# Kernel tuning notes

Measured on AMD Instinct MI355X. Metric: run time of the kernel, lower is better.

Reference implementation:

```python
import jax, jax.numpy as jnp
import numpy as np

N_NODES = 50000
N_EDGES = 800000
IN_CH = 128
H1, C1 = 8, 16      # conv1: 8 heads x 16 channels, concat -> 128
H2, C2 = 1, 64      # conv2: 1 head x 64 channels, mean (concat=False)
NEG_SLOPE = 0.2


def setup_inputs() -> dict:
    key = jax.random.key(0)
    ks = jax.random.split(key, 10)
    x = jax.random.normal(ks[0], (N_NODES, IN_CH), dtype=jnp.float32)
    edge_index = jax.random.randint(ks[1], (2, N_EDGES), 0, N_NODES, dtype=jnp.int64)
    s1 = 1.0 / np.sqrt(IN_CH)
    s2 = 1.0 / np.sqrt(H1 * C1)
    W1 = jax.random.normal(ks[2], (IN_CH, H1 * C1), dtype=jnp.float32) * s1
    att_src1 = jax.random.normal(ks[3], (H1, C1), dtype=jnp.float32) * s1
    att_dst1 = jax.random.normal(ks[4], (H1, C1), dtype=jnp.float32) * s1
    b1 = jnp.zeros((H1 * C1,), dtype=jnp.float32)
    W2 = jax.random.normal(ks[5], (H1 * C1, H2 * C2), dtype=jnp.float32) * s2
    att_src2 = jax.random.normal(ks[6], (H2, C2), dtype=jnp.float32) * s2
    att_dst2 = jax.random.normal(ks[7], (H2, C2), dtype=jnp.float32) * s2
    b2 = jnp.zeros((C2,), dtype=jnp.float32)
    return {"x": x, "edge_index": edge_index, "W1": W1, "att_src1": att_src1,
            "att_dst1": att_dst1, "b1": b1, "W2": W2, "att_src2": att_src2,
            "att_dst2": att_dst2, "b2": b2}


def gat_conv(x, src, dst, W, att_src, att_dst, bias, heads, out_ch, concat):
    # x: [N, F_in]; src/dst: [E'] (self-loops already appended)
    N = x.shape[0]
    h = (x @ W).reshape(N, heads, out_ch)                     # [N, H, C]
    a_s = jnp.sum(h * att_src[None], axis=-1)                 # [N, H]
    a_d = jnp.sum(h * att_dst[None], axis=-1)                 # [N, H]
    logits = jax.nn.leaky_relu(a_s[src] + a_d[dst], NEG_SLOPE)  # [E', H]
    # segment softmax over edges grouped by destination node
    m = jax.ops.segment_max(logits, dst, num_segments=N)       # [N, H]
    e = jnp.exp(logits - m[dst])                               # [E', H]
    denom = jax.ops.segment_sum(e, dst, num_segments=N)        # [N, H]
    alpha = e / (denom[dst] + 1e-16)                           # [E', H]
    msg = h[src] * alpha[:, :, None]                           # [E', H, C]
    out = jax.ops.segment_sum(msg, dst, num_segments=N)        # [N, H, C]
    if concat:
        out = out.reshape(N, heads * out_ch)
    else:
        out = out.mean(axis=1)
    return out + bias


def reference(x, edge_index, W1, att_src1, att_dst1, b1, W2, att_src2, att_dst2, b2):
    N = x.shape[0]
    loop = jnp.arange(N, dtype=edge_index.dtype)
    src = jnp.concatenate([edge_index[0], loop])   # GATConv adds self-loops
    dst = jnp.concatenate([edge_index[1], loop])
    # eval mode: all dropouts are identity
    h = gat_conv(x, src, dst, W1, att_src1, att_dst1, b1, H1, C1, concat=True)
    h = jax.nn.elu(h)
    out = gat_conv(h, src, dst, W2, att_src2, att_dst2, b2, H2, C2, concat=False)
    return jax.nn.log_softmax(out, axis=1)
```

## Files before the change

kernel.cpp:

```cpp
#include <hip/hip_runtime.h>
#include <math.h>

#define IN_CH 128
#define H1N 8
#define C1N 16
#define C2N 64
#define NEG_SLOPE 0.2f

#define BKT_SHIFT 7
#define BKT_NODES (1 << BKT_SHIFT)
#define NBLK 128

typedef unsigned short ushortT;

__device__ __forceinline__ ushortT f2bf(float f) {
    unsigned u = __float_as_uint(f);
    unsigned r = u + 0x7FFFu + ((u >> 16) & 1u);
    return (ushortT)(r >> 16);
}
__device__ __forceinline__ float bf2f(ushortT b) {
    return __uint_as_float(((unsigned)b) << 16);
}
__device__ __forceinline__ float leaky(float x) {
    return (x > 0.f) ? x : NEG_SLOPE * x;
}


__global__ __launch_bounds__(512) void k_cnt(const int* __restrict__ src,
                                             const int* __restrict__ dst,
                                             int E, int N, int* __restrict__ cnt) {
    __shared__ int hist[512];
    int blk = blockIdx.x, t = threadIdx.x;
    int nb = (N + BKT_NODES - 1) >> BKT_SHIFT;
    if (t < nb) hist[t] = 0;
    __syncthreads();
    int Etot = E + N;
    int chunk = (Etot + gridDim.x - 1) / gridDim.x;
    int lo = blk * chunk;
    int hi = lo + chunk; if (hi > Etot) hi = Etot;
    for (int i = lo + t; i < hi; i += 512) {
        int d = (i < E) ? dst[i] : (i - E);
        atomicAdd(&hist[d >> BKT_SHIFT], 1);
    }
    __syncthreads();
    if (t < nb) cnt[t * NBLK + blk] = hist[t];
}

__global__ __launch_bounds__(NBLK) void k_scanrel(int* __restrict__ cnt,
                                                  int* __restrict__ bucketTotal) {
    __shared__ int sh[NBLK];
    int b = blockIdx.x, t = threadIdx.x;
    sh[t] = cnt[b * NBLK + t];
    __syncthreads();
    for (int off = 1; off < NBLK; off <<= 1) {
        int v = (t >= off) ? sh[t - off] : 0;
        __syncthreads();
        sh[t] += v;
        __syncthreads();
    }
    if (t == NBLK - 1) bucketTotal[b] = sh[t];
    cnt[b * NBLK + t] = (t == 0) ? 0 : sh[t - 1];
}

__global__ __launch_bounds__(512) void k_scanbucket(const int* __restrict__ bucketTotal,
                                                    int nb, int* __restrict__ bBase,
                                                    int N, int* __restrict__ offsets) {
    __shared__ int sh[512];
    int t = threadIdx.x;
    sh[t] = (t < nb) ? bucketTotal[t] : 0;
    __syncthreads();
    for (int off = 1; off < 512; off <<= 1) {
        int v = (t >= off) ? sh[t - off] : 0;
        __syncthreads();
        sh[t] += v;
        __syncthreads();
    }
    if (t < nb) bBase[t] = (t == 0) ? 0 : sh[t - 1];
    if (t == 511) { bBase[nb] = sh[511]; offsets[N] = sh[511]; }
}

__global__ __launch_bounds__(512) void k_bin(const int* __restrict__ src,
                                             const int* __restrict__ dst,
                                             int E, int N,
                                             const int* __restrict__ cnt,
                                             const int* __restrict__ bBase,
                                             unsigned* __restrict__ pair) {
    __shared__ int cur[512];
    int blk = blockIdx.x, t = threadIdx.x;
    int nb = (N + BKT_NODES - 1) >> BKT_SHIFT;
    if (t < nb) cur[t] = bBase[t] + cnt[t * NBLK + blk];
    __syncthreads();
    int Etot = E + N;
    int chunk = (Etot + gridDim.x - 1) / gridDim.x;
    int lo = blk * chunk;
    int hi = lo + chunk; if (hi > Etot) hi = Etot;
    for (int i = lo + t; i < hi; i += 512) {
        int s, d;
        if (i < E) { s = src[i]; d = dst[i]; }
        else       { s = d = i - E; }
        int b = d >> BKT_SHIFT;
        int pos = atomicAdd(&cur[b], 1);
        pair[pos] = ((unsigned)(d & (BKT_NODES - 1)) << 16) | (unsigned)s;
    }
}

__global__ __launch_bounds__(256) void k_csr_local(const unsigned* __restrict__ pair,
                                                   const int* __restrict__ bBase,
                                                   int N, int* __restrict__ offsets,
                                                   ushortT* __restrict__ csr) {
    __shared__ int hist[BKT_NODES];
    __shared__ int loff[BKT_NODES];
    int b = blockIdx.x;
    int t = threadIdx.x;
    int base = bBase[b];
    int cnt = bBase[b + 1] - base;
    const unsigned* pp = pair + base;

    if (t < BKT_NODES) hist[t] = 0;
    __syncthreads();
    for (int i = t; i < cnt; i += 256) atomicAdd(&hist[pp[i] >> 16], 1);
    __syncthreads();
    if (t < BKT_NODES) loff[t] = hist[t];
    __syncthreads();
    for (int off = 1; off < BKT_NODES; off <<= 1) {
        int v = 0;
        if (t < BKT_NODES && t >= off) v = loff[t - off];
        __syncthreads();
        if (t < BKT_NODES) loff[t] += v;
        __syncthreads();
    }
    int node0 = b << BKT_SHIFT;
    if (t < BKT_NODES) {
        int excl = (t == 0) ? 0 : loff[t - 1];
        hist[t] = excl;
        int g = node0 + t;
        if (g < N) offsets[g] = base + excl;
    }
    __syncthreads();
    for (int i = t; i < cnt; i += 256) {
        unsigned pk = pp[i];
        int pos = atomicAdd(&hist[pk >> 16], 1);
        csr[base + pos] = (ushortT)(pk & 0xFFFFu);
    }
}


template <int KOUT, int HEADS>
__global__ __launch_bounds__(256) void k_gemm_att(const float* __restrict__ A,
                                                  const float* __restrict__ W,
                                                  const float* __restrict__ att_s,
                                                  const float* __restrict__ att_d,
                                                  int N, ushortT* __restrict__ Cbf,
                                                  float* __restrict__ as_,
                                                  float* __restrict__ ad_) {
    constexpr int CG  = KOUT / 4;
    constexpr int TY  = 256 / CG;
    constexpr int RPT = 64 / TY;
    constexpr int RW  = (KOUT / HEADS) / 4;
    static_assert(RW == 4 || RW == 16, "reduce width");
    __shared__ float As[64][16];
    __shared__ float Ws[16][KOUT];
    int t = threadIdx.x;
    int row0 = blockIdx.x * 64;
    int tx = t % CG, ty = t / CG;

    float4 acc[RPT];
#pragma unroll
    for (int i = 0; i < RPT; ++i) acc[i] = make_float4(0.f, 0.f, 0.f, 0.f);

    for (int k0 = 0; k0 < IN_CH; k0 += 16) {
        {
            int r  = t >> 2;
            int cc = (t & 3) * 4;
            int gr = row0 + r;
            float4 v = make_float4(0.f, 0.f, 0.f, 0.f);
            if (gr < N) v = *(const float4*)(A + (size_t)gr * IN_CH + k0 + cc);
            *(float4*)(&As[r][cc]) = v;
        }
        {
            constexpr int TOT = 16 * KOUT / 4;
            for (int idx = t; idx < TOT; idx += 256) {
                int rr = idx / (KOUT / 4);
                int cc = (idx % (KOUT / 4)) * 4;
                *(float4*)(&Ws[rr][cc]) = *(const float4*)(W + (size_t)(k0 + rr) * KOUT + cc);
            }
        }
        __syncthreads();
#pragma unroll
        for (int kk = 0; kk < 16; ++kk) {
            float4 w = *(const float4*)(&Ws[kk][tx * 4]);
#pragma unroll
            for (int i = 0; i < RPT; ++i) {
                float a = As[ty * RPT + i][kk];
                acc[i].x += a * w.x; acc[i].y += a * w.y;
                acc[i].z += a * w.z; acc[i].w += a * w.w;
            }
        }
        __syncthreads();
    }

    float4 s4 = *(const float4*)(att_s + tx * 4);
    float4 d4 = *(const float4*)(att_d + tx * 4);
#pragma unroll
    for (int i = 0; i < RPT; ++i) {
        int gr = row0 + ty * RPT + i;
        float as = acc[i].x * s4.x + acc[i].y * s4.y + acc[i].z * s4.z + acc[i].w * s4.w;
        float ad = acc[i].x * d4.x + acc[i].y * d4.y + acc[i].z * d4.z + acc[i].w * d4.w;
#pragma unroll
        for (int o = 1; o < RW; o <<= 1) {
            as += __shfl_xor(as, o);
            ad += __shfl_xor(ad, o);
        }
        if (gr < N) {
            ushort4 pk;
            pk.x = f2bf(acc[i].x); pk.y = f2bf(acc[i].y);
            pk.z = f2bf(acc[i].z); pk.w = f2bf(acc[i].w);
            *(ushort4*)(Cbf + (size_t)gr * KOUT + tx * 4) = pk;
            if ((tx % RW) == 0) {
                int h = tx / RW;
                as_[(size_t)gr * HEADS + h] = as;
                ad_[(size_t)gr * HEADS + h] = ad;
            }
        }
    }
}


__global__ void k_agg1(const ushortT* __restrict__ h1bf,
                       const float* __restrict__ as1, const float* __restrict__ ad1,
                       const int* __restrict__ offsets, const ushortT* __restrict__ csr,
                       const float* __restrict__ b1,
                       int N, float* __restrict__ h2in) {
    int wid  = (blockIdx.x * blockDim.x + threadIdx.x) >> 6;
    int lane = threadIdx.x & 63;
    if (wid >= N) return;
    int v = wid;
    int hc = lane >> 3;
    int hp = lane & 7;
    float adc = ad1[v * H1N + hc];
    float adp = ad1[v * H1N + hp];
    float denom = 0.f, acc0 = 0.f, acc1 = 0.f;
    int beg = offsets[v], end = offsets[v + 1];
    int j = beg;
    for (; j + 8 <= end; j += 8) {
        int ep = lane >> 3;
        int sE = csr[j + ep];
        float a = as1[sE * H1N + hp];
        float pp = __expf(leaky(a + adp));
#pragma unroll
        for (int e = 0; e < 8; ++e) {
            int srcl = e * 8 + hc;
            float pe = __shfl(pp, srcl);
            int   se = __shfl(sE, srcl);
            unsigned q = *(const unsigned*)(h1bf + (size_t)se * IN_CH + lane * 2);
            denom += pe;
            acc0 = fmaf(pe, bf2f((ushortT)(q & 0xFFFFu)), acc0);
            acc1 = fmaf(pe, bf2f((ushortT)(q >> 16)), acc1);
        }
    }
    if (j + 4 <= end) {
        int ep = (lane >> 3) & 3;
        int sE = csr[j + ep];
        float a = as1[sE * H1N + hp];
        float pp = __expf(leaky(a + adp));
#pragma unroll
        for (int e = 0; e < 4; ++e) {
            int srcl = e * 8 + hc;
            float pe = __shfl(pp, srcl);
            int   se = __shfl(sE, srcl);
            unsigned q = *(const unsigned*)(h1bf + (size_t)se * IN_CH + lane * 2);
            denom += pe;
            acc0 = fmaf(pe, bf2f((ushortT)(q & 0xFFFFu)), acc0);
            acc1 = fmaf(pe, bf2f((ushortT)(q >> 16)), acc1);
        }
        j += 4;
    }
    for (; j < end; ++j) {
        int s = csr[j];
        float a = as1[s * H1N + hc];
        unsigned q = *(const unsigned*)(h1bf + (size_t)s * IN_CH + lane * 2);
        float p = __expf(leaky(a + adc));
        denom += p;
        acc0 = fmaf(p, bf2f((ushortT)(q & 0xFFFFu)), acc0);
        acc1 = fmaf(p, bf2f((ushortT)(q >> 16)), acc1);
    }
    float inv = 1.f / (denom + 1e-16f);
    float o0 = acc0 * inv + b1[lane * 2];
    float o1 = acc1 * inv + b1[lane * 2 + 1];
    o0 = (o0 > 0.f) ? o0 : expm1f(o0);
    o1 = (o1 > 0.f) ? o1 : expm1f(o1);
    float2 ov; ov.x = o0; ov.y = o1;
    *(float2*)(h2in + (size_t)v * IN_CH + lane * 2) = ov;
}


__global__ void k_agg2(const ushortT* __restrict__ h2bf,
                       const float* __restrict__ as2, const float* __restrict__ ad2,
                       const int* __restrict__ offsets, const ushortT* __restrict__ csr,
                       const float* __restrict__ b2,
                       int N, float* __restrict__ out) {
    int wid  = (blockIdx.x * blockDim.x + threadIdx.x) >> 6;
    int lane = threadIdx.x & 63;
    if (wid >= N) return;
    int v = wid;
    float ad = ad2[v];
    float denom = 0.f, acc = 0.f;
    int beg = offsets[v], end = offsets[v + 1];
    int j = beg;
    for (; j + 8 <= end; j += 8) {
        int ep = lane & 7;
        int sE = csr[j + ep];
        float pp = __expf(leaky(as2[sE] + ad));
#pragma unroll
        for (int e = 0; e < 8; ++e) {
            float pe = __shfl(pp, e);
            int   se = __shfl(sE, e);
            float x = bf2f(h2bf[(size_t)se * C2N + lane]);
            denom += pe;
            acc = fmaf(pe, x, acc);
        }
    }
    for (; j < end; ++j) {
        int s = csr[j];
        float p = __expf(leaky(as2[s] + ad));
        float x = bf2f(h2bf[(size_t)s * C2N + lane]);
        denom += p;
        acc = fmaf(p, x, acc);
    }
    float o = acc / (denom + 1e-16f) + b2[lane];
    float mx = o;
#pragma unroll
    for (int off = 32; off >= 1; off >>= 1) mx = fmaxf(mx, __shfl_xor(mx, off));
    float e = __expf(o - mx);
    float se = e;
#pragma unroll
    for (int off = 32; off >= 1; off >>= 1) se += __shfl_xor(se, off);
    out[(size_t)v * C2N + lane] = o - mx - logf(se);
}


extern "C" void kernel_launch(void* const* d_in, const int* in_sizes, int n_in,
                              void* d_out, int out_size, void* d_ws, size_t ws_size,
                              hipStream_t stream) {
    const float* x      = (const float*)d_in[0];
    const int*   ei     = (const int*)d_in[1];
    const float* W1     = (const float*)d_in[2];
    const float* att_s1 = (const float*)d_in[3];
    const float* att_d1 = (const float*)d_in[4];
    const float* b1     = (const float*)d_in[5];
    const float* W2     = (const float*)d_in[6];
    const float* att_s2 = (const float*)d_in[7];
    const float* att_d2 = (const float*)d_in[8];
    const float* b2     = (const float*)d_in[9];

    int N = in_sizes[0] / IN_CH;
    int E = in_sizes[1] / 2;
    const int* srcA = ei;
    const int* dstA = ei + E;
    int Etot = E + N;
    int nb = (N + BKT_NODES - 1) >> BKT_SHIFT;

    char* p = (char*)d_ws;
    auto carve = [&](size_t bytes) {
        void* r = (void*)p;
        p += (bytes + 255) & ~(size_t)255;
        return r;
    };
    ushortT* h1bf = (ushortT*)carve((size_t)N * IN_CH * 2);
    ushortT* h2bf = (ushortT*)carve((size_t)N * C2N * 2);
    float* h2in = (float*)carve((size_t)N * IN_CH * 4);
    float* as1  = (float*)carve((size_t)N * H1N * 4);
    float* ad1  = (float*)carve((size_t)N * H1N * 4);
    float* as2  = (float*)carve((size_t)N * 4);
    float* ad2  = (float*)carve((size_t)N * 4);
    int* offsets     = (int*)carve((size_t)(N + 1) * 4);
    ushortT* csr     = (ushortT*)carve((size_t)Etot * 2);
    int* cnt         = (int*)carve((size_t)nb * NBLK * 4);
    int* bucketTotal = (int*)carve((size_t)nb * 4);
    int* bBase       = (int*)carve((size_t)(nb + 1) * 4);
    unsigned* pair   = (unsigned*)carve((size_t)Etot * 4);

    k_cnt<<<NBLK, 512, 0, stream>>>(srcA, dstA, E, N, cnt);
    k_scanrel<<<nb, NBLK, 0, stream>>>(cnt, bucketTotal);
    k_scanbucket<<<1, 512, 0, stream>>>(bucketTotal, nb, bBase, N, offsets);
    k_bin<<<NBLK, 512, 0, stream>>>(srcA, dstA, E, N, cnt, bBase, pair);
    k_csr_local<<<nb, 256, 0, stream>>>(pair, bBase, N, offsets, csr);

    k_gemm_att<128, 8><<<(N + 63) / 64, 256, 0, stream>>>(x, W1, att_s1, att_d1,
                                                          N, h1bf, as1, ad1);
    k_agg1<<<(N * 64 + 255) / 256, 256, 0, stream>>>(h1bf, as1, ad1, offsets, csr, b1, N, h2in);

    k_gemm_att<64, 1><<<(N + 63) / 64, 256, 0, stream>>>(h2in, W2, att_s2, att_d2,
                                                         N, h2bf, as2, ad2);
    k_agg2<<<(N * 64 + 255) / 256, 256, 0, stream>>>(h2bf, as2, ad2, offsets, csr, b2, N, (float*)d_out);
}
```

Before: 164.9 us.

## Split each node's edge aggregation across two wavefronts with LDS combine

```diff
diff --git a/kernel.cpp b/kernel.cpp
--- a/kernel.cpp
+++ b/kernel.cpp
@@ -226,31 +226,41 @@
 }
 
 
-__global__ void k_agg1(const ushortT* __restrict__ h1bf,
+__global__ __launch_bounds__(256) void k_agg1(const ushortT* __restrict__ h1bf,
                        const float* __restrict__ as1, const float* __restrict__ ad1,
                        const int* __restrict__ offsets, const ushortT* __restrict__ csr,
                        const float* __restrict__ b1,
                        int N, float* __restrict__ h2in) {
-    int wid  = (blockIdx.x * blockDim.x + threadIdx.x) >> 6;
-    int lane = threadIdx.x & 63;
-    if (wid >= N) return;
-    int v = wid;
+    __shared__ float comb[2][192];
+    int t = threadIdx.x;
+    int half = t >> 7;
+    int wv   = (t >> 6) & 1;
+    int lane = t & 63;
+    int v = blockIdx.x * 2 + half;
+    bool alive = (v < N);
+
     int hc = lane >> 3;
     int hp = lane & 7;
-    float adc = ad1[v * H1N + hc];
-    float adp = ad1[v * H1N + hp];
+    int ep = lane >> 3;
+    float adp = 0.f;
+    int beg = 0, end = 0;
+    if (alive) {
+        adp = ad1[v * H1N + hp];
+        beg = offsets[v];
+        end = offsets[v + 1];
+    }
     float denom = 0.f, acc0 = 0.f, acc1 = 0.f;
-    int beg = offsets[v], end = offsets[v + 1];
-    int j = beg;
-    for (; j + 8 <= end; j += 8) {
-        int ep = lane >> 3;
-        int sE = csr[j + ep];
-        float a = as1[sE * H1N + hp];
-        float pp = __expf(leaky(a + adp));
-#pragma unroll
-        for (int e = 0; e < 8; ++e) {
+    for (int j = beg + wv * 8; j < end; j += 16) {
+        int m = end - j; if (m > 8) m = 8;
+        int sE = 0;
+        float p = 0.f;
+        if (ep < m) {
+            sE = csr[j + ep];
+            p = __expf(leaky(as1[sE * H1N + hp] + adp));
+        }
+        for (int e = 0; e < m; ++e) {
             int srcl = e * 8 + hc;
-            float pe = __shfl(pp, srcl);
+            float pe = __shfl(p, srcl);
             int   se = __shfl(sE, srcl);
             unsigned q = *(const unsigned*)(h1bf + (size_t)se * IN_CH + lane * 2);
             denom += pe;
@@ -258,84 +268,83 @@
             acc1 = fmaf(pe, bf2f((ushortT)(q >> 16)), acc1);
         }
     }
-    if (j + 4 <= end) {
-        int ep = (lane >> 3) & 3;
-        int sE = csr[j + ep];
-        float a = as1[sE * H1N + hp];
-        float pp = __expf(leaky(a + adp));
-#pragma unroll
-        for (int e = 0; e < 4; ++e) {
-            int srcl = e * 8 + hc;
-            float pe = __shfl(pp, srcl);
-            int   se = __shfl(sE, srcl);
-            unsigned q = *(const unsigned*)(h1bf + (size_t)se * IN_CH + lane * 2);
-            denom += pe;
-            acc0 = fmaf(pe, bf2f((ushortT)(q & 0xFFFFu)), acc0);
-            acc1 = fmaf(pe, bf2f((ushortT)(q >> 16)), acc1);
-        }
-        j += 4;
-    }
-    for (; j < end; ++j) {
-        int s = csr[j];
-        float a = as1[s * H1N + hc];
-        unsigned q = *(const unsigned*)(h1bf + (size_t)s * IN_CH + lane * 2);
-        float p = __expf(leaky(a + adc));
-        denom += p;
-        acc0 = fmaf(p, bf2f((ushortT)(q & 0xFFFFu)), acc0);
-        acc1 = fmaf(p, bf2f((ushortT)(q >> 16)), acc1);
-    }
-    float inv = 1.f / (denom + 1e-16f);
-    float o0 = acc0 * inv + b1[lane * 2];
-    float o1 = acc1 * inv + b1[lane * 2 + 1];
-    o0 = (o0 > 0.f) ? o0 : expm1f(o0);
-    o1 = (o1 > 0.f) ? o1 : expm1f(o1);
-    float2 ov; ov.x = o0; ov.y = o1;
-    *(float2*)(h2in + (size_t)v * IN_CH + lane * 2) = ov;
-}
-
-
-__global__ void k_agg2(const ushortT* __restrict__ h2bf,
+    if (wv == 1) {
+        comb[half][lane * 2]     = acc0;
+        comb[half][lane * 2 + 1] = acc1;
+        comb[half][128 + lane]   = denom;
+    }
+    __syncthreads();
+    if (wv == 0 && alive) {
+        acc0  += comb[half][lane * 2];
+        acc1  += comb[half][lane * 2 + 1];
+        denom += comb[half][128 + lane];
+        float inv = 1.f / (denom + 1e-16f);
+        float o0 = acc0 * inv + b1[lane * 2];
+        float o1 = acc1 * inv + b1[lane * 2 + 1];
+        o0 = (o0 > 0.f) ? o0 : expm1f(o0);
+        o1 = (o1 > 0.f) ? o1 : expm1f(o1);
+        float2 ov; ov.x = o0; ov.y = o1;
+        *(float2*)(h2in + (size_t)v * IN_CH + lane * 2) = ov;
+    }
+}
+
+
+__global__ __launch_bounds__(256) void k_agg2(const ushortT* __restrict__ h2bf,
                        const float* __restrict__ as2, const float* __restrict__ ad2,
                        const int* __restrict__ offsets, const ushortT* __restrict__ csr,
                        const float* __restrict__ b2,
                        int N, float* __restrict__ out) {
-    int wid  = (blockIdx.x * blockDim.x + threadIdx.x) >> 6;
-    int lane = threadIdx.x & 63;
-    if (wid >= N) return;
-    int v = wid;
-    float ad = ad2[v];
+    __shared__ float comb[2][128];
+    int t = threadIdx.x;
+    int half = t >> 7;
+    int wv   = (t >> 6) & 1;
+    int lane = t & 63;
+    int v = blockIdx.x * 2 + half;
+    bool alive = (v < N);
+
+    float ad = 0.f;
+    int beg = 0, end = 0;
+    if (alive) {
+        ad = ad2[v];
+        beg = offsets[v];
+        end = offsets[v + 1];
+    }
     float denom = 0.f, acc = 0.f;
-    int beg = offsets[v], end = offsets[v + 1];
-    int j = beg;
-    for (; j + 8 <= end; j += 8) {
+    for (int j = beg + wv * 8; j < end; j += 16) {
+        int m = end - j; if (m > 8) m = 8;
         int ep = lane & 7;
-        int sE = csr[j + ep];
-        float pp = __expf(leaky(as2[sE] + ad));
-#pragma unroll
-        for (int e = 0; e < 8; ++e) {
-            float pe = __shfl(pp, e);
+        int sE = 0;
+        float p = 0.f;
+        if (ep < m) {
+            sE = csr[j + ep];
+            p = __expf(leaky(as2[sE] + ad));
+        }
+        for (int e = 0; e < m; ++e) {
+            float pe = __shfl(p, e);
             int   se = __shfl(sE, e);
             float x = bf2f(h2bf[(size_t)se * C2N + lane]);
             denom += pe;
             acc = fmaf(pe, x, acc);
         }
     }
-    for (; j < end; ++j) {
-        int s = csr[j];
-        float p = __expf(leaky(as2[s] + ad));
-        float x = bf2f(h2bf[(size_t)s * C2N + lane]);
-        denom += p;
-        acc = fmaf(p, x, acc);
-    }
-    float o = acc / (denom + 1e-16f) + b2[lane];
-    float mx = o;
-#pragma unroll
-    for (int off = 32; off >= 1; off >>= 1) mx = fmaxf(mx, __shfl_xor(mx, off));
-    float e = __expf(o - mx);
-    float se = e;
-#pragma unroll
-    for (int off = 32; off >= 1; off >>= 1) se += __shfl_xor(se, off);
-    out[(size_t)v * C2N + lane] = o - mx - logf(se);
+    if (wv == 1) {
+        comb[half][lane]      = acc;
+        comb[half][64 + lane] = denom;
+    }
+    __syncthreads();
+    if (wv == 0 && alive) {
+        acc   += comb[half][lane];
+        denom += comb[half][64 + lane];
+        float o = acc / (denom + 1e-16f) + b2[lane];
+        float mx = o;
+#pragma unroll
+        for (int off = 32; off >= 1; off >>= 1) mx = fmaxf(mx, __shfl_xor(mx, off));
+        float e = __expf(o - mx);
+        float se = e;
+#pragma unroll
+        for (int off = 32; off >= 1; off >>= 1) se += __shfl_xor(se, off);
+        out[(size_t)v * C2N + lane] = o - mx - logf(se);
+    }
 }
 
 
@@ -388,9 +397,9 @@
 
     k_gemm_att<128, 8><<<(N + 63) / 64, 256, 0, stream>>>(x, W1, att_s1, att_d1,
                                                           N, h1bf, as1, ad1);
-    k_agg1<<<(N * 64 + 255) / 256, 256, 0, stream>>>(h1bf, as1, ad1, offsets, csr, b1, N, h2in);
+    k_agg1<<<(N + 1) / 2, 256, 0, stream>>>(h1bf, as1, ad1, offsets, csr, b1, N, h2in);
 
     k_gemm_att<64, 1><<<(N + 63) / 64, 256, 0, stream>>>(h2in, W2, att_s2, att_d2,
                                                          N, h2bf, as2, ad2);
-    k_agg2<<<(N * 64 + 255) / 256, 256, 0, stream>>>(h2bf, as2, ad2, offsets, csr, b2, N, (float*)d_out);
-}
+    k_agg2<<<(N + 1) / 2, 256, 0, stream>>>(h2bf, as2, ad2, offsets, csr, b2, N, (float*)d_out);
+}
```

Result: slower. 243.7 us (+47.8%).

## Precompute per-edge attention exponentials in separate edge-parallel kernels

Applied to the files above, without the earlier changes.

```diff
diff --git a/kernel.cpp b/kernel.cpp
--- a/kernel.cpp
+++ b/kernel.cpp
@@ -12,6 +12,7 @@
 #define NBLK 128
 
 typedef unsigned short ushortT;
+typedef unsigned char ucharT;
 
 __device__ __forceinline__ ushortT f2bf(float f) {
     unsigned u = __float_as_uint(f);
@@ -107,7 +108,8 @@
 __global__ __launch_bounds__(256) void k_csr_local(const unsigned* __restrict__ pair,
                                                    const int* __restrict__ bBase,
                                                    int N, int* __restrict__ offsets,
-                                                   ushortT* __restrict__ csr) {
+                                                   ushortT* __restrict__ csr,
+                                                   ucharT* __restrict__ dloc) {
     __shared__ int hist[BKT_NODES];
     __shared__ int loff[BKT_NODES];
     int b = blockIdx.x;
@@ -139,8 +141,10 @@
     __syncthreads();
     for (int i = t; i < cnt; i += 256) {
         unsigned pk = pp[i];
-        int pos = atomicAdd(&hist[pk >> 16], 1);
-        csr[base + pos] = (ushortT)(pk & 0xFFFFu);
+        int dl = pk >> 16;
+        int pos = atomicAdd(&hist[dl], 1);
+        csr[base + pos]  = (ushortT)(pk & 0xFFFFu);
+        dloc[base + pos] = (ucharT)dl;
     }
 }
 
@@ -226,63 +230,91 @@
 }
 
 
-__global__ void k_agg1(const ushortT* __restrict__ h1bf,
-                       const float* __restrict__ as1, const float* __restrict__ ad1,
+__global__ __launch_bounds__(256) void k_pexp1(const ushortT* __restrict__ csr,
+                                               const ucharT* __restrict__ dloc,
+                                               const int* __restrict__ bBase,
+                                               const float* __restrict__ as1,
+                                               const float* __restrict__ ad1,
+                                               int N, int Etot,
+                                               ushortT* __restrict__ p1T) {
+    __shared__ float ad1s[BKT_NODES * H1N];
+    int b = blockIdx.x, t = threadIdx.x;
+    int node0 = b << BKT_SHIFT;
+    for (int i = t; i < BKT_NODES * H1N; i += 256) {
+        int g = node0 + (i >> 3);
+        ad1s[i] = (g < N) ? ad1[(size_t)g * H1N + (i & 7)] : 0.f;
+    }
+    __syncthreads();
+    int base = bBase[b];
+    int cnt  = bBase[b + 1] - base;
+#pragma unroll
+    for (int h = 0; h < H1N; ++h) {
+        for (int i = t; i < cnt; i += 256) {
+            int s  = csr[base + i];
+            int dl = dloc[base + i];
+            float a = as1[(size_t)s * H1N + h] + ad1s[dl * H1N + h];
+            p1T[(size_t)h * Etot + base + i] = f2bf(__expf(leaky(a)));
+        }
+    }
+}
+
+__global__ __launch_bounds__(256) void k_pexp2(const ushortT* __restrict__ csr,
+                                               const ucharT* __restrict__ dloc,
+                                               const int* __restrict__ bBase,
+                                               const float* __restrict__ as2,
+                                               const float* __restrict__ ad2,
+                                               int N,
+                                               ushortT* __restrict__ p2) {
+    __shared__ float ad2s[BKT_NODES];
+    int b = blockIdx.x, t = threadIdx.x;
+    int node0 = b << BKT_SHIFT;
+    if (t < BKT_NODES) {
+        int g = node0 + t;
+        ad2s[t] = (g < N) ? ad2[g] : 0.f;
+    }
+    __syncthreads();
+    int base = bBase[b];
+    int cnt  = bBase[b + 1] - base;
+    for (int i = t; i < cnt; i += 256) {
+        int s  = csr[base + i];
+        int dl = dloc[base + i];
+        p2[base + i] = f2bf(__expf(leaky(as2[s] + ad2s[dl])));
+    }
+}
+
+
+__global__ __launch_bounds__(256) void k_agg1(const ushortT* __restrict__ h1bf,
+                       const ushortT* __restrict__ p1T,
                        const int* __restrict__ offsets, const ushortT* __restrict__ csr,
                        const float* __restrict__ b1,
-                       int N, float* __restrict__ h2in) {
+                       int N, int Etot, float* __restrict__ h2in) {
     int wid  = (blockIdx.x * blockDim.x + threadIdx.x) >> 6;
     int lane = threadIdx.x & 63;
     if (wid >= N) return;
     int v = wid;
     int hc = lane >> 3;
-    int hp = lane & 7;
-    float adc = ad1[v * H1N + hc];
-    float adp = ad1[v * H1N + hp];
+    const ushortT* pT = p1T + (size_t)hc * Etot;
     float denom = 0.f, acc0 = 0.f, acc1 = 0.f;
     int beg = offsets[v], end = offsets[v + 1];
     int j = beg;
     for (; j + 8 <= end; j += 8) {
-        int ep = lane >> 3;
-        int sE = csr[j + ep];
-        float a = as1[sE * H1N + hp];
-        float pp = __expf(leaky(a + adp));
 #pragma unroll
         for (int e = 0; e < 8; ++e) {
-            int srcl = e * 8 + hc;
-            float pe = __shfl(pp, srcl);
-            int   se = __shfl(sE, srcl);
+            int se = csr[j + e];
+            float pe = bf2f(pT[j + e]);
             unsigned q = *(const unsigned*)(h1bf + (size_t)se * IN_CH + lane * 2);
             denom += pe;
             acc0 = fmaf(pe, bf2f((ushortT)(q & 0xFFFFu)), acc0);
             acc1 = fmaf(pe, bf2f((ushortT)(q >> 16)), acc1);
         }
     }
-    if (j + 4 <= end) {
-        int ep = (lane >> 3) & 3;
-        int sE = csr[j + ep];
-        float a = as1[sE * H1N + hp];
-        float pp = __expf(leaky(a + adp));
-#pragma unroll
-        for (int e = 0; e < 4; ++e) {
-            int srcl = e * 8 + hc;
-            float pe = __shfl(pp, srcl);
-            int   se = __shfl(sE, srcl);
-            unsigned q = *(const unsigned*)(h1bf + (size_t)se * IN_CH + lane * 2);
-            denom += pe;
-            acc0 = fmaf(pe, bf2f((ushortT)(q & 0xFFFFu)), acc0);
-            acc1 = fmaf(pe, bf2f((ushortT)(q >> 16)), acc1);
-        }
-        j += 4;
-    }
     for (; j < end; ++j) {
-        int s = csr[j];
-        float a = as1[s * H1N + hc];
-        unsigned q = *(const unsigned*)(h1bf + (size_t)s * IN_CH + lane * 2);
-        float p = __expf(leaky(a + adc));
-        denom += p;
-        acc0 = fmaf(p, bf2f((ushortT)(q & 0xFFFFu)), acc0);
-        acc1 = fmaf(p, bf2f((ushortT)(q >> 16)), acc1);
+        int se = csr[j];
+        float pe = bf2f(pT[j]);
+        unsigned q = *(const unsigned*)(h1bf + (size_t)se * IN_CH + lane * 2);
+        denom += pe;
+        acc0 = fmaf(pe, bf2f((ushortT)(q & 0xFFFFu)), acc0);
+        acc1 = fmaf(pe, bf2f((ushortT)(q >> 16)), acc1);
     }
     float inv = 1.f / (denom + 1e-16f);
     float o0 = acc0 * inv + b1[lane * 2];
@@ -294,8 +326,8 @@
 }
 
 
-__global__ void k_agg2(const ushortT* __restrict__ h2bf,
-                       const float* __restrict__ as2, const float* __restrict__ ad2,
+__global__ __launch_bounds__(256) void k_agg2(const ushortT* __restrict__ h2bf,
+                       const ushortT* __restrict__ p2,
                        const int* __restrict__ offsets, const ushortT* __restrict__ csr,
                        const float* __restrict__ b2,
                        int N, float* __restrict__ out) {
@@ -303,29 +335,25 @@
     int lane = threadIdx.x & 63;
     if (wid >= N) return;
     int v = wid;
-    float ad = ad2[v];
     float denom = 0.f, acc = 0.f;
     int beg = offsets[v], end = offsets[v + 1];
     int j = beg;
     for (; j + 8 <= end; j += 8) {
-        int ep = lane & 7;
-        int sE = csr[j + ep];
-        float pp = __expf(leaky(as2[sE] + ad));
 #pragma unroll
         for (int e = 0; e < 8; ++e) {
-            float pe = __shfl(pp, e);
-            int   se = __shfl(sE, e);
+            int se = csr[j + e];
+            float pe = bf2f(p2[j + e]);
             float x = bf2f(h2bf[(size_t)se * C2N + lane]);
             denom += pe;
             acc = fmaf(pe, x, acc);
         }
     }
     for (; j < end; ++j) {
-        int s = csr[j];
-        float p = __expf(leaky(as2[s] + ad));
-        float x = bf2f(h2bf[(size_t)s * C2N + lane]);
-        denom += p;
-        acc = fmaf(p, x, acc);
+        int se = csr[j];
+        float pe = bf2f(p2[j]);
+        float x = bf2f(h2bf[(size_t)se * C2N + lane]);
+        denom += pe;
+        acc = fmaf(pe, x, acc);
     }
     float o = acc / (denom + 1e-16f) + b2[lane];
     float mx = o;
@@ -375,22 +403,29 @@
     float* ad2  = (float*)carve((size_t)N * 4);
     int* offsets     = (int*)carve((size_t)(N + 1) * 4);
     ushortT* csr     = (ushortT*)carve((size_t)Etot * 2);
+    ucharT* dloc     = (ucharT*)carve((size_t)Etot);
     int* cnt         = (int*)carve((size_t)nb * NBLK * 4);
     int* bucketTotal = (int*)carve((size_t)nb * 4);
     int* bBase       = (int*)carve((size_t)(nb + 1) * 4);
     unsigned* pair   = (unsigned*)carve((size_t)Etot * 4);
+    ushortT* p1T     = (ushortT*)carve((size_t)H1N * Etot * 2);
+    ushortT* p2      = (ushortT*)carve((size_t)Etot * 2);
 
     k_cnt<<<NBLK, 512, 0, stream>>>(srcA, dstA, E, N, cnt);
     k_scanrel<<<nb, NBLK, 0, stream>>>(cnt, bucketTotal);
     k_scanbucket<<<1, 512, 0, stream>>>(bucketTotal, nb, bBase, N, offsets);
     k_bin<<<NBLK, 512, 0, stream>>>(srcA, dstA, E, N, cnt, bBase, pair);
-    k_csr_local<<<nb, 256, 0, stream>>>(pair, bBase, N, offsets, csr);
+    k_csr_local<<<nb, 256, 0, stream>>>(pair, bBase, N, offsets, csr, dloc);
 
     k_gemm_att<128, 8><<<(N + 63) / 64, 256, 0, stream>>>(x, W1, att_s1, att_d1,
                                                           N, h1bf, as1, ad1);
-    k_agg1<<<(N * 64 + 255) / 256, 256, 0, stream>>>(h1bf, as1, ad1, offsets, csr, b1, N, h2in);
+    k_pexp1<<<nb, 256, 0, stream>>>(csr, dloc, bBase, as1, ad1, N, Etot, p1T);
+    k_agg1<<<(N * 64 + 255) / 256, 256, 0, stream>>>(h1bf, p1T, offsets, csr, b1,
+                                                     N, Etot, h2in);
 
     k_gemm_att<64, 1><<<(N + 63) / 64, 256, 0, stream>>>(h2in, W2, att_s2, att_d2,
                                                          N, h2bf, as2, ad2);
-    k_agg2<<<(N * 64 + 255) / 256, 256, 0, stream>>>(h2bf, as2, ad2, offsets, csr, b2, N, (float*)d_out);
-}
+    k_pexp2<<<nb, 256, 0, stream>>>(csr, dloc, bBase, as2, ad2, N, p2);
+    k_agg2<<<(N * 64 + 255) / 256, 256, 0, stream>>>(h2bf, p2, offsets, csr, b2,
+                                                     N, (float*)d_out);
+}
```

New measurement: 214.7 us. 1.3x slower.

## Store layer-1 output in bf16 and process two nodes per wavefront in agg2

Applied to the files above, without the earlier changes.

```diff
diff --git a/kernel.cpp b/kernel.cpp
--- a/kernel.cpp
+++ b/kernel.cpp
@@ -145,8 +145,8 @@
 }
 
 
-template <int KOUT, int HEADS>
-__global__ __launch_bounds__(256) void k_gemm_att(const float* __restrict__ A,
+template <int KOUT, int HEADS, bool BFIN>
+__global__ __launch_bounds__(256) void k_gemm_att(const void* __restrict__ Av,
                                                   const float* __restrict__ W,
                                                   const float* __restrict__ att_s,
                                                   const float* __restrict__ att_d,
@@ -174,7 +174,16 @@
             int cc = (t & 3) * 4;
             int gr = row0 + r;
             float4 v = make_float4(0.f, 0.f, 0.f, 0.f);
-            if (gr < N) v = *(const float4*)(A + (size_t)gr * IN_CH + k0 + cc);
+            if (gr < N) {
+                if constexpr (BFIN) {
+                    const ushortT* A = (const ushortT*)Av;
+                    ushort4 u = *(const ushort4*)(A + (size_t)gr * IN_CH + k0 + cc);
+                    v.x = bf2f(u.x); v.y = bf2f(u.y); v.z = bf2f(u.z); v.w = bf2f(u.w);
+                } else {
+                    const float* A = (const float*)Av;
+                    v = *(const float4*)(A + (size_t)gr * IN_CH + k0 + cc);
+                }
+            }
             *(float4*)(&As[r][cc]) = v;
         }
         {
@@ -230,7 +239,7 @@
                        const float* __restrict__ as1, const float* __restrict__ ad1,
                        const int* __restrict__ offsets, const ushortT* __restrict__ csr,
                        const float* __restrict__ b1,
-                       int N, float* __restrict__ h2in) {
+                       int N, ushortT* __restrict__ h2in) {
     int wid  = (blockIdx.x * blockDim.x + threadIdx.x) >> 6;
     int lane = threadIdx.x & 63;
     if (wid >= N) return;
@@ -289,53 +298,79 @@
     float o1 = acc1 * inv + b1[lane * 2 + 1];
     o0 = (o0 > 0.f) ? o0 : expm1f(o0);
     o1 = (o1 > 0.f) ? o1 : expm1f(o1);
-    float2 ov; ov.x = o0; ov.y = o1;
-    *(float2*)(h2in + (size_t)v * IN_CH + lane * 2) = ov;
-}
-
-
-__global__ void k_agg2(const ushortT* __restrict__ h2bf,
+    unsigned pk = ((unsigned)f2bf(o1) << 16) | (unsigned)f2bf(o0);
+    *(unsigned*)(h2in + (size_t)v * IN_CH + lane * 2) = pk;
+}
+
+
+__global__ __launch_bounds__(256) void k_agg2(const ushortT* __restrict__ h2bf,
                        const float* __restrict__ as2, const float* __restrict__ ad2,
                        const int* __restrict__ offsets, const ushortT* __restrict__ csr,
                        const float* __restrict__ b2,
                        int N, float* __restrict__ out) {
     int wid  = (blockIdx.x * blockDim.x + threadIdx.x) >> 6;
     int lane = threadIdx.x & 63;
-    if (wid >= N) return;
-    int v = wid;
-    float ad = ad2[v];
-    float denom = 0.f, acc = 0.f;
-    int beg = offsets[v], end = offsets[v + 1];
+    int half = lane >> 5;
+    int v = wid * 2 + half;
+    bool alive = (v < N);
+    int c2 = (lane & 31) * 2;
+
+    float ad = 0.f;
+    int beg = 0, end = 0;
+    if (alive) {
+        ad = ad2[v];
+        beg = offsets[v];
+        end = offsets[v + 1];
+    }
+    float denom = 0.f, acc0 = 0.f, acc1 = 0.f;
     int j = beg;
     for (; j + 8 <= end; j += 8) {
+        int sE = csr[j + (lane & 7)];
+        float p = __expf(leaky(as2[sE] + ad));
+#pragma unroll
+        for (int e = 0; e < 8; ++e) {
+            int srcl = (lane & 32) + e;
+            float pe = __shfl(p, srcl);
+            int   se = __shfl(sE, srcl);
+            unsigned q = *(const unsigned*)(h2bf + (size_t)se * C2N + c2);
+            denom += pe;
+            acc0 = fmaf(pe, bf2f((ushortT)(q & 0xFFFFu)), acc0);
+            acc1 = fmaf(pe, bf2f((ushortT)(q >> 16)), acc1);
+        }
+    }
+    if (j < end) {
+        int m = end - j;
         int ep = lane & 7;
-        int sE = csr[j + ep];
-        float pp = __expf(leaky(as2[sE] + ad));
-#pragma unroll
-        for (int e = 0; e < 8; ++e) {
-            float pe = __shfl(pp, e);
-            int   se = __shfl(sE, e);
-            float x = bf2f(h2bf[(size_t)se * C2N + lane]);
+        int sE = 0;
+        float p = 0.f;
+        if (ep < m) {
+            sE = csr[j + ep];
+            p = __expf(leaky(as2[sE] + ad));
+        }
+        for (int e = 0; e < m; ++e) {
+            int srcl = (lane & 32) + e;
+            float pe = __shfl(p, srcl);
+            int   se = __shfl(sE, srcl);
+            unsigned q = *(const unsigned*)(h2bf + (size_t)se * C2N + c2);
             denom += pe;
-            acc = fmaf(pe, x, acc);
-        }
-    }
-    for (; j < end; ++j) {
-        int s = csr[j];
-        float p = __expf(leaky(as2[s] + ad));
-        float x = bf2f(h2bf[(size_t)s * C2N + lane]);
-        denom += p;
-        acc = fmaf(p, x, acc);
-    }
-    float o = acc / (denom + 1e-16f) + b2[lane];
-    float mx = o;
-#pragma unroll
-    for (int off = 32; off >= 1; off >>= 1) mx = fmaxf(mx, __shfl_xor(mx, off));
-    float e = __expf(o - mx);
-    float se = e;
-#pragma unroll
-    for (int off = 32; off >= 1; off >>= 1) se += __shfl_xor(se, off);
-    out[(size_t)v * C2N + lane] = o - mx - logf(se);
+            acc0 = fmaf(pe, bf2f((ushortT)(q & 0xFFFFu)), acc0);
+            acc1 = fmaf(pe, bf2f((ushortT)(q >> 16)), acc1);
+        }
+    }
+    float inv = 1.f / (denom + 1e-16f);
+    float o0 = acc0 * inv + b2[c2];
+    float o1 = acc1 * inv + b2[c2 + 1];
+    float mx = fmaxf(o0, o1);
+#pragma unroll
+    for (int off = 16; off >= 1; off >>= 1) mx = fmaxf(mx, __shfl_xor(mx, off));
+    float se2 = __expf(o0 - mx) + __expf(o1 - mx);
+#pragma unroll
+    for (int off = 16; off >= 1; off >>= 1) se2 += __shfl_xor(se2, off);
+    if (alive) {
+        float lse = logf(se2);
+        float2 ov; ov.x = o0 - mx - lse; ov.y = o1 - mx - lse;
+        *(float2*)(out + (size_t)v * C2N + c2) = ov;
+    }
 }
 
 
@@ -368,13 +403,13 @@
     };
     ushortT* h1bf = (ushortT*)carve((size_t)N * IN_CH * 2);
     ushortT* h2bf = (ushortT*)carve((size_t)N * C2N * 2);
-    float* h2in = (float*)carve((size_t)N * IN_CH * 4);
+    ushortT* h2in = (ushortT*)carve((size_t)N * IN_CH * 2);
     float* as1  = (float*)carve((size_t)N * H1N * 4);
     float* ad1  = (float*)carve((size_t)N * H1N * 4);
     float* as2  = (float*)carve((size_t)N * 4);
     float* ad2  = (float*)carve((size_t)N * 4);
     int* offsets     = (int*)carve((size_t)(N + 1) * 4);
-    ushortT* csr     = (ushortT*)carve((size_t)Etot * 2);
+    ushortT* csr     = (ushortT*)carve((size_t)(Etot + 16) * 2);
     int* cnt         = (int*)carve((size_t)nb * NBLK * 4);
     int* bucketTotal = (int*)carve((size_t)nb * 4);
     int* bBase       = (int*)carve((size_t)(nb + 1) * 4);
@@ -386,11 +421,12 @@
     k_bin<<<NBLK, 512, 0, stream>>>(srcA, dstA, E, N, cnt, bBase, pair);
     k_csr_local<<<nb, 256, 0, stream>>>(pair, bBase, N, offsets, csr);
 
-    k_gemm_att<128, 8><<<(N + 63) / 64, 256, 0, stream>>>(x, W1, att_s1, att_d1,
-                                                          N, h1bf, as1, ad1);
+    k_gemm_att<128, 8, false><<<(N + 63) / 64, 256, 0, stream>>>(x, W1, att_s1, att_d1,
+                                                                 N, h1bf, as1, ad1);
     k_agg1<<<(N * 64 + 255) / 256, 256, 0, stream>>>(h1bf, as1, ad1, offsets, csr, b1, N, h2in);
 
-    k_gemm_att<64, 1><<<(N + 63) / 64, 256, 0, stream>>>(h2in, W2, att_s2, att_d2,
-                                                         N, h2bf, as2, ad2);
-    k_agg2<<<(N * 64 + 255) / 256, 256, 0, stream>>>(h2bf, as2, ad2, offsets, csr, b2, N, (float*)d_out);
-}
+    k_gemm_att<64, 1, true><<<(N + 63) / 64, 256, 0, stream>>>(h2in, W2, att_s2, att_d2,
+                                                               N, h2bf, as2, ad2);
+    k_agg2<<<(N * 32 + 255) / 256, 256, 0, stream>>>(h2bf, as2, ad2, offsets, csr, b2,
+                                                     N, (float*)d_out);
+}
```

Measured after the change: 148.7 us. -9.8%, faster.
